# Optimization experiments

Measured on AMD Instinct MI355X. Metric: run time of the kernel, lower is better.

The kernel has to match this reference:

```python
import jax, jax.numpy as jnp
import numpy as np

IMG = 640.0
FISHER_EPS = 1e-6
BN_EPS = 1e-5
K = 100  # num_proposals

def _conv(x, w, b, stride=1, pad=1):
    y = jax.lax.conv_general_dilated(x, w, (stride, stride), [(pad, pad), (pad, pad)],
                                     dimension_numbers=('NCHW', 'OIHW', 'NCHW'))
    return y + b[None, :, None, None]

def _bn(x, g, b):
    # eval-mode BatchNorm, running_mean=0, running_var=1
    scale = g / np.float32(np.sqrt(1.0 + BN_EPS))
    return x * scale[None, :, None, None] + b[None, :, None, None]

def _lin(x, w, b):
    return jnp.einsum('...i,oi->...o', x, w) + b

def _gelu(x):
    return jax.nn.gelu(x, approximate=False)

def setup_inputs():
    key = jax.random.key(0)
    ks = iter(jax.random.split(key, 64))
    def W(shape, s=0.05):
        return (jax.random.normal(next(ks), shape) * s).astype(jnp.float32)
    Z = lambda n: jnp.zeros((n,), jnp.float32)
    O = lambda n: jnp.ones((n,), jnp.float32)
    return dict(
        images=jax.random.normal(next(ks), (8, 3, 640, 640), jnp.float32),
        enc_w1=W((32, 3, 3, 3)), enc_b1=Z(32), bn1_g=O(32), bn1_b=Z(32),
        enc_w2=W((64, 32, 3, 3)), enc_b2=Z(64), bn2_g=O(64), bn2_b=Z(64),
        enc_w3=W((128, 64, 3, 3)), enc_b3=Z(128), bn3_g=O(128), bn3_b=Z(128),
        dist_w1=W((64, 128, 3, 3)), dist_b1=Z(64), dist_w2=W((15, 64, 1, 1)), dist_b2=Z(15),
        feat_w=W((128, 128, 3, 3)), feat_b=Z(128), bnf_g=O(128), bnf_b=Z(128),
        temperature=jnp.array(1.0, jnp.float32),
        score_w1=W((64, 129, 3, 3)), score_b1=Z(64), score_w2=W((1, 64, 1, 1)), score_b2=Z(1),
        det_w=W((128, 128)), det_b=Z(128),
        co_w1=W((32, 128)), co_b1=Z(32), co_w2=W((2, 32)), co_b2=Z(2),
        sz_w1=W((32, 128)), sz_b1=Z(32), sz_w2=W((2, 32)), sz_b2=Z(2),
        an_w1=W((16, 128)), an_b1=Z(16), an_w2=W((1, 16)), an_b2=Z(1),
        cls_w1=W((64, 128)), cls_b1=Z(64), cls_w2=W((15, 64)), cls_b2=Z(15),
        conf_w1=W((16, 129)), conf_b1=Z(16), conf_w2=W((1, 16)), conf_b2=Z(1),
    )

def reference(images, enc_w1, enc_b1, bn1_g, bn1_b, enc_w2, enc_b2, bn2_g, bn2_b,
              enc_w3, enc_b3, bn3_g, bn3_b, dist_w1, dist_b1, dist_w2, dist_b2,
              feat_w, feat_b, bnf_g, bnf_b, temperature,
              score_w1, score_b1, score_w2, score_b2, det_w, det_b,
              co_w1, co_b1, co_w2, co_b2, sz_w1, sz_b1, sz_w2, sz_b2,
              an_w1, an_b1, an_w2, an_b2, cls_w1, cls_b1, cls_w2, cls_b2,
              conf_w1, conf_b1, conf_w2, conf_b2):
    # FisherEncoder
    x = _gelu(_bn(_conv(images, enc_w1, enc_b1, stride=2), bn1_g, bn1_b))
    x = _gelu(_bn(_conv(x, enc_w2, enc_b2, stride=2), bn2_g, bn2_b))
    enc = _gelu(_bn(_conv(x, enc_w3, enc_b3), bn3_g, bn3_b))
    logits = _conv(jax.nn.relu(_conv(enc, dist_w1, dist_b1)), dist_w2, dist_b2, pad=0)
    features = _gelu(_bn(_conv(enc, feat_w, feat_b), bnf_g, bnf_b))
    # DiagonalFisherModule (analytical; num_fisher_samples=0)
    temp = jnp.clip(temperature, 0.1, 10.0)
    probs = jax.nn.sigmoid(logits / temp)
    fisher_map = jnp.maximum(probs * (1.0 - probs), FISHER_EPS).sum(axis=1, keepdims=True)
    # score refinement
    score_in = jnp.concatenate([features, fisher_map], axis=1)
    scores_map = jax.nn.sigmoid(_conv(jax.nn.relu(_conv(score_in, score_w1, score_b1)), score_w2, score_b2, pad=0))
    B, C, H, W = features.shape
    N = H * W
    top_scores, top_idx = jax.lax.top_k(scores_map.reshape(B, N), K)  # (B,K)
    ys = (top_idx // W).astype(jnp.float32) / H
    xs = (top_idx % W).astype(jnp.float32) / W
    coords = jnp.stack([xs, ys], axis=-1)  # (B,K,2)
    # gather per-proposal features
    local = jnp.take_along_axis(features.reshape(B, C, N), top_idx[:, None, :], axis=2)  # (B,C,K)
    local = jnp.transpose(local, (0, 2, 1))  # (B,K,C)
    feat = jax.nn.relu(_lin(local, det_w, det_b))
    offsets = jnp.tanh(_lin(jax.nn.relu(_lin(feat, co_w1, co_b1)), co_w2, co_b2))
    offset_scale = jnp.array([1.0 / W, 1.0 / H], jnp.float32)
    centers = (coords + offsets * offset_scale) * IMG
    wh = jnp.exp(jnp.clip(_lin(jax.nn.relu(_lin(feat, sz_w1, sz_b1)), sz_w2, sz_b2), -5.0, 5.0)) * (IMG / 10.0)
    a = _lin(jax.nn.relu(_lin(feat, an_w1, an_b1)), an_w2, an_b2)
    angles = jnp.arctan2(jnp.sin(a), jnp.cos(a))
    cls_logits = _lin(jax.nn.relu(_lin(feat, cls_w1, cls_b1)), cls_w2, cls_b2)
    conf_in = jnp.concatenate([feat, top_scores[..., None]], axis=-1)
    conf = jax.nn.sigmoid(_lin(jax.nn.relu(_lin(conf_in, conf_w1, conf_b1)), conf_w2, conf_b2))
    return (centers, wh, angles, cls_logits, conf, top_scores, fisher_map)
```

## Files before the change

### kernel.cpp

```cpp
#include <hip/hip_runtime.h>
#include <cmath>

#define ACT_NONE 0
#define ACT_GELU 1
#define ACT_RELU 2

#define OFF_CENTERS 0
#define OFF_WH      1600
#define OFF_ANG     3200
#define OFF_CLS     4000
#define OFF_CONF    16000
#define OFF_TOPS    16800
#define OFF_FISH    17600

__device__ __forceinline__ float gelu_f(float v) {
    return 0.5f * v * (1.f + erff(v * 0.70710678118654752f));
}

__global__ void prep_weight(const float* __restrict__ w, const float* __restrict__ bn_g,
                            float* __restrict__ wt, int O, int I9) {
    int i = blockIdx.x * 256 + threadIdx.x;
    if (i >= O * I9) return;
    int o = i / I9, r = i % I9;
    float s = 1.f;
    if (bn_g) {
        double sq = sqrt(1.0 + 1e-5);
        s = bn_g[o] / (float)sq;
    }
    wt[(size_t)r * O + o] = w[(size_t)o * I9 + r] * s;
}

__global__ void prep_bias(const float* __restrict__ b, const float* __restrict__ bn_g,
                          const float* __restrict__ bn_b, float* __restrict__ outb, int O) {
    int o = blockIdx.x * 128 + threadIdx.x;
    if (o >= O) return;
    float s = 1.f, t = 0.f;
    if (bn_g) {
        double sq = sqrt(1.0 + 1e-5);
        s = bn_g[o] / (float)sq;
        t = bn_b[o];
    }
    outb[o] = b[o] * s + t;
}

__global__ void zero_cols_k(float* __restrict__ buf, int nplanes, int W, int H) {
    int i = blockIdx.x * 256 + threadIdx.x;
    if (i >= nplanes * H * 2) return;
    const int p = i / (H * 2), j = i % (H * 2);
    const int y = j >> 1, side = j & 1;
    buf[(size_t)p * W * H + (size_t)y * W + (side ? W - 1 : 0)] = 0.f;
}

__global__ void zero_fill_k(float* __restrict__ buf, int n) {
    int i = blockIdx.x * 256 + threadIdx.x;
    if (i < n) buf[i] = 0.f;
}

template<int CIN, int COUT, int CHUNK, int STRIDE, int HOUT, int WOUT, int ACT, bool OPADX>
__global__ __launch_bounds__(256) void conv3x3_k(
    const float* __restrict__ in, const float* __restrict__ wt,
    const float* __restrict__ bias, float* __restrict__ out)
{
    constexpr int HIN = HOUT * STRIDE, WIN = WOUT * STRIDE;
    constexpr int NCH = COUT / CHUNK;
    const int tx = threadIdx.x & 15, ty = threadIdx.x >> 4;
    const int x = blockIdx.x * 16 + tx;
    const int y = blockIdx.y * 16 + ty;
    const int b = blockIdx.z / NCH;
    const int co0 = (blockIdx.z % NCH) * CHUNK;

    float acc[CHUNK];
#pragma unroll
    for (int c = 0; c < CHUNK; ++c) acc[c] = bias[co0 + c];

    const float* inb = in + (size_t)b * CIN * HIN * WIN;
#pragma unroll 1
    for (int ci = 0; ci < CIN; ++ci) {
        const float* ip = inb + (size_t)ci * HIN * WIN;
#pragma unroll
        for (int ky = 0; ky < 3; ++ky) {
            const int iy = y * STRIDE + ky - 1;
            const bool yok = (unsigned)iy < (unsigned)HIN;
#pragma unroll
            for (int kx = 0; kx < 3; ++kx) {
                const int ix = x * STRIDE + kx - 1;
                const bool ok = yok && ((unsigned)ix < (unsigned)WIN);
                const float v = ok ? ip[(size_t)iy * WIN + ix] : 0.f;
                const float* wp = wt + ((size_t)(ci * 9 + ky * 3 + kx)) * COUT + co0;
#pragma unroll
                for (int c = 0; c < CHUNK; ++c) acc[c] = fmaf(v, wp[c], acc[c]);
            }
        }
    }
#pragma unroll
    for (int c = 0; c < CHUNK; ++c) {
        float v = acc[c];
        if (ACT == ACT_GELU) v = gelu_f(v);
        if (ACT == ACT_RELU) v = fmaxf(v, 0.f);
        if (OPADX) {
            out[((size_t)b * COUT + co0 + c) * (size_t)(HOUT * (WOUT + 2))
                + (size_t)y * (WOUT + 2) + (x + 1)] = v;
        } else {
            out[((size_t)b * COUT + co0 + c) * (size_t)(HOUT * WOUT)
                + (size_t)y * WOUT + x] = v;
        }
    }
}

#define FMA16(A, V, W0, W1, W2, W3) do { \
  A[0]=fmaf((V),(W0).x,A[0]); A[1]=fmaf((V),(W0).y,A[1]); A[2]=fmaf((V),(W0).z,A[2]); A[3]=fmaf((V),(W0).w,A[3]); \
  A[4]=fmaf((V),(W1).x,A[4]); A[5]=fmaf((V),(W1).y,A[5]); A[6]=fmaf((V),(W1).z,A[6]); A[7]=fmaf((V),(W1).w,A[7]); \
  A[8]=fmaf((V),(W2).x,A[8]); A[9]=fmaf((V),(W2).y,A[9]); A[10]=fmaf((V),(W2).z,A[10]); A[11]=fmaf((V),(W2).w,A[11]); \
  A[12]=fmaf((V),(W3).x,A[12]); A[13]=fmaf((V),(W3).y,A[13]); A[14]=fmaf((V),(W3).z,A[14]); A[15]=fmaf((V),(W3).w,A[15]); \
} while (0)

template<int CIN, int COUT, int S, int PW, int HIN, int ACT, bool EXTRA, bool OPAD>
__global__ __launch_bounds__(256) void conv4_k(
    const float* __restrict__ in, const float* __restrict__ extra,
    const float* __restrict__ wt, const float* __restrict__ bias,
    const float* __restrict__ zrow, float* __restrict__ out)
{
    constexpr int PPIN = HIN * PW;
    constexpr int CHUNK = 16, NCH = COUT / CHUNK;
    constexpr int CTOT = CIN + (EXTRA ? 1 : 0);
    constexpr int NL = 3 * S + 3;
    const int tx = threadIdx.x & 7, ty = threadIdx.x >> 3;
    const int ox0 = blockIdx.x * 32 + tx * 4;
    const int oy  = blockIdx.y * 32 + ty;
    const int b   = blockIdx.z / NCH;
    const int co0 = (blockIdx.z % NCH) * CHUNK;

    float acc[4][16];
#pragma unroll
    for (int c = 0; c < 16; ++c) {
        const float bv = bias[co0 + c];
#pragma unroll
        for (int p = 0; p < 4; ++p) acc[p][c] = bv;
    }

    int rowoff[3], rok[3];
#pragma unroll
    for (int r = 0; r < 3; ++r) {
        const int riy = oy * S + r - 1;
        rok[r] = (riy >= 0 && riy < HIN) ? 1 : 0;
        const int rr = riy < 0 ? 0 : (riy >= HIN ? HIN - 1 : riy);
        rowoff[r] = rr * PW + ox0 * S;
    }

    const float* inb = in + (size_t)b * CIN * PPIN;
    const float* wb  = wt + co0;

#pragma unroll 1
    for (int ci = 0; ci < CTOT; ++ci) {
        const float* chp = (EXTRA && ci == CIN) ? (extra + (size_t)b * PPIN)
                                                : (inb + (size_t)ci * PPIN);
        float v[3][NL];
#pragma unroll
        for (int r = 0; r < 3; ++r) {
            const float* pr = rok[r] ? (chp + rowoff[r]) : zrow;
#pragma unroll
            for (int j = 0; j < NL / 2; ++j) {
                const float2 t = *(const float2*)(pr + 2 * j);
                v[r][2 * j] = t.x; v[r][2 * j + 1] = t.y;
            }
            if (NL & 1) v[r][NL - 1] = pr[NL - 1];
        }
        const float* wr = wb + (size_t)(ci * 9) * COUT;
#pragma unroll
        for (int ky = 0; ky < 3; ++ky) {
#pragma unroll
            for (int kx = 0; kx < 3; ++kx) {
                const float* wp = wr + (size_t)(ky * 3 + kx) * COUT;
                const float4 w0 = *(const float4*)(wp);
                const float4 w1 = *(const float4*)(wp + 4);
                const float4 w2 = *(const float4*)(wp + 8);
                const float4 w3 = *(const float4*)(wp + 12);
#pragma unroll
                for (int p = 0; p < 4; ++p) {
                    const float a = v[ky][p * S + kx];
                    FMA16(acc[p], a, w0, w1, w2, w3);
                }
            }
        }
    }

#pragma unroll
    for (int c = 0; c < 16; ++c) {
#pragma unroll
        for (int p = 0; p < 4; ++p) {
            float u = acc[p][c];
            if (ACT == ACT_GELU) u = gelu_f(u);
            if (ACT == ACT_RELU) u = fmaxf(u, 0.f);
            if (OPAD) {
                out[((size_t)b * COUT + co0 + c) * (160 * 162)
                    + (size_t)oy * 162 + (ox0 + p + 1)] = u;
            } else {
                out[((size_t)b * COUT + co0 + c) * (160 * 160)
                    + (size_t)oy * 160 + (ox0 + p)] = u;
            }
        }
    }
}

__global__ __launch_bounds__(256) void dist2_fisher_k(
    const float* __restrict__ hid, const float* __restrict__ w ,
    const float* __restrict__ b2 , const float* __restrict__ temp,
    float* __restrict__ fisher_out, float* __restrict__ fisher_pad)
{
    const int p = blockIdx.x * 256 + threadIdx.x;
    if (p >= 8 * 25600) return;
    const int bi = p / 25600, pix = p % 25600;
    const float* h = hid + (size_t)bi * 64 * 25600 + pix;
    float hv[64];
#pragma unroll
    for (int i = 0; i < 64; ++i) hv[i] = h[(size_t)i * 25600];
    const float t = fminf(fmaxf(temp[0], 0.1f), 10.f);
    const float inv_t = 1.f / t;
    float fsum = 0.f;
#pragma unroll 1
    for (int c = 0; c < 15; ++c) {
        float l = b2[c];
        const float* wr = w + c * 64;
#pragma unroll
        for (int i = 0; i < 64; ++i) l = fmaf(hv[i], wr[i], l);
        const float pr = 1.f / (1.f + expf(-l * inv_t));
        fsum += fmaxf(pr * (1.f - pr), 1e-6f);
    }
    fisher_out[p] = fsum;
    const int yy = pix / 160, xx = pix % 160;
    fisher_pad[(size_t)bi * (160 * 162) + (size_t)yy * 162 + (xx + 1)] = fsum;
}

__global__ __launch_bounds__(256) void score2_k(
    const float* __restrict__ hid, const float* __restrict__ w ,
    const float* __restrict__ b, float* __restrict__ sc)
{
    const int p = blockIdx.x * 256 + threadIdx.x;
    if (p >= 8 * 25600) return;
    const int bi = p / 25600, pix = p % 25600;
    const float* h = hid + (size_t)bi * 64 * 25600 + pix;
    float a = b[0];
#pragma unroll
    for (int i = 0; i < 64; ++i) a = fmaf(h[(size_t)i * 25600], w[i], a);
    sc[p] = 1.f / (1.f + expf(-a));
}

#define TK_CAP 512
__global__ __launch_bounds__(256) void topk_radix_k(
    const float* __restrict__ scores, float* __restrict__ topv, int* __restrict__ topi)
{
    __shared__ unsigned hist[256];
    __shared__ unsigned gv[128]; __shared__ int gi[128];
    __shared__ unsigned ecnt[2];
    __shared__ int ei_[TK_CAP];
    __shared__ unsigned fv[100]; __shared__ int fi[100];
    __shared__ unsigned sel_prefix; __shared__ int sel_remaining;
    const int b = blockIdx.x, t = threadIdx.x;
    const float* s = scores + (size_t)b * 25600;

    unsigned prefix = 0; int remaining = 100;
    for (int pass = 0; pass < 4; ++pass) {
        const int shift = 24 - 8 * pass;
        hist[t] = 0;
        __syncthreads();
        const unsigned pmask = (pass == 0) ? 0u : (0xFFFFFFFFu << (shift + 8));
        for (int i = t; i < 25600; i += 256) {
            const unsigned k = __float_as_uint(s[i]);
            if ((k & pmask) == prefix)
                atomicAdd(&hist[(k >> shift) & 255], 1u);
        }
        __syncthreads();
        if (t == 0) {
            unsigned cum = 0; int bkt = 0;
            for (int d = 255; d >= 0; --d) {
                const unsigned c = hist[d];
                if (cum + c >= (unsigned)remaining) { bkt = d; break; }
                cum += c;
            }
            sel_prefix = prefix | ((unsigned)bkt << shift);
            sel_remaining = remaining - (int)cum;
        }
        __syncthreads();
        prefix = sel_prefix; remaining = sel_remaining;
        __syncthreads();
    }
    if (t == 0) { ecnt[0] = 0; ecnt[1] = 0; }
    __syncthreads();
    for (int i = t; i < 25600; i += 256) {
        const unsigned k = __float_as_uint(s[i]);
        if (k > prefix) {
            const unsigned p = atomicAdd(&ecnt[0], 1u);
            gv[p] = k; gi[p] = i;
        } else if (k == prefix) {
            const unsigned p = atomicAdd(&ecnt[1], 1u);
            if (p < TK_CAP) ei_[p] = i;
        }
    }
    __syncthreads();
    const int cG = (int)ecnt[0];
    const int cE = (int)ecnt[1] < TK_CAP ? (int)ecnt[1] : TK_CAP;
    if (t < cG) { fv[t] = gv[t]; fi[t] = gi[t]; }
    if (t < cE) {
        const int idx = ei_[t]; int r = 0;
        for (int l = 0; l < cE; ++l) r += (ei_[l] < idx) ? 1 : 0;
        if (r < remaining) { fv[cG + r] = prefix; fi[cG + r] = idx; }
    }
    __syncthreads();
    if (t < 100) {
        const unsigned myv = fv[t]; const int myi = fi[t]; int r = 0;
        for (int l = 0; l < 100; ++l) {
            const unsigned v = fv[l]; const int li = fi[l];
            r += (v > myv || (v == myv && li < myi)) ? 1 : 0;
        }
        topv[b * 100 + r] = __uint_as_float(myv);
        topi[b * 100 + r] = myi;
    }
}

__global__ __launch_bounds__(128) void heads_k(
    const float* __restrict__ features, const float* __restrict__ topv,
    const int* __restrict__ topi,
    const float* __restrict__ det_w, const float* __restrict__ det_b,
    const float* __restrict__ co_w1, const float* __restrict__ co_b1,
    const float* __restrict__ co_w2, const float* __restrict__ co_b2,
    const float* __restrict__ sz_w1, const float* __restrict__ sz_b1,
    const float* __restrict__ sz_w2, const float* __restrict__ sz_b2,
    const float* __restrict__ an_w1, const float* __restrict__ an_b1,
    const float* __restrict__ an_w2, const float* __restrict__ an_b2,
    const float* __restrict__ cls_w1, const float* __restrict__ cls_b1,
    const float* __restrict__ cls_w2, const float* __restrict__ cls_b2,
    const float* __restrict__ conf_w1, const float* __restrict__ conf_b1,
    const float* __restrict__ conf_w2, const float* __restrict__ conf_b2,
    float* __restrict__ out)
{
    __shared__ float local[128], feat[128], h[64];
    const int bk = blockIdx.x;
    const int b = bk / 100;
    const int t = threadIdx.x;
    const int idx = topi[bk];
    const float score = topv[bk];

    const int yy = idx / 160, xx = idx % 160;
    local[t] = features[((size_t)b * 128 + t) * (160 * 162) + (size_t)yy * 162 + (xx + 1)];
    __syncthreads();

    {
        float a = det_b[t];
        const float* wr = det_w + (size_t)t * 128;
#pragma unroll
        for (int i = 0; i < 128; ++i) a = fmaf(local[i], wr[i], a);
        feat[t] = fmaxf(a, 0.f);
    }
    __syncthreads();

    if (t < 32) {
        float a = co_b1[t];
        const float* wr = co_w1 + (size_t)t * 128;
#pragma unroll
        for (int i = 0; i < 128; ++i) a = fmaf(feat[i], wr[i], a);
        h[t] = fmaxf(a, 0.f);
    }
    __syncthreads();
    if (t < 2) {
        float a = co_b2[t];
        const float* wr = co_w2 + (size_t)t * 32;
#pragma unroll
        for (int j = 0; j < 32; ++j) a = fmaf(h[j], wr[j], a);
        const float off = tanhf(a);
        const float coord = (t == 0) ? (float)xx * (1.f / 160.f) : (float)yy * (1.f / 160.f);
        out[OFF_CENTERS + bk * 2 + t] = (coord + off * (1.f / 160.f)) * 640.f;
    }
    __syncthreads();

    if (t < 32) {
        float a = sz_b1[t];
        const float* wr = sz_w1 + (size_t)t * 128;
#pragma unroll
        for (int i = 0; i < 128; ++i) a = fmaf(feat[i], wr[i], a);
        h[t] = fmaxf(a, 0.f);
    }
    __syncthreads();
    if (t < 2) {
        float a = sz_b2[t];
        const float* wr = sz_w2 + (size_t)t * 32;
#pragma unroll
        for (int j = 0; j < 32; ++j) a = fmaf(h[j], wr[j], a);
        a = fminf(fmaxf(a, -5.f), 5.f);
        out[OFF_WH + bk * 2 + t] = expf(a) * 64.f;
    }
    __syncthreads();

    if (t < 16) {
        float a = an_b1[t];
        const float* wr = an_w1 + (size_t)t * 128;
#pragma unroll
        for (int i = 0; i < 128; ++i) a = fmaf(feat[i], wr[i], a);
        h[t] = fmaxf(a, 0.f);
    }
    __syncthreads();
    if (t == 0) {
        float a = an_b2[0];
#pragma unroll
        for (int j = 0; j < 16; ++j) a = fmaf(h[j], an_w2[j], a);
        out[OFF_ANG + bk] = atan2f(sinf(a), cosf(a));
    }
    __syncthreads();

    if (t < 64) {
        float a = cls_b1[t];
        const float* wr = cls_w1 + (size_t)t * 128;
#pragma unroll
        for (int i = 0; i < 128; ++i) a = fmaf(feat[i], wr[i], a);
        h[t] = fmaxf(a, 0.f);
    }
    __syncthreads();
    if (t < 15) {
        float a = cls_b2[t];
        const float* wr = cls_w2 + (size_t)t * 64;
#pragma unroll
        for (int j = 0; j < 64; ++j) a = fmaf(h[j], wr[j], a);
        out[OFF_CLS + bk * 15 + t] = a;
    }
    __syncthreads();

    if (t < 16) {
        float a = conf_b1[t];
        const float* wr = conf_w1 + (size_t)t * 129;
#pragma unroll
        for (int i = 0; i < 128; ++i) a = fmaf(feat[i], wr[i], a);
        a = fmaf(score, wr[128], a);
        h[t] = fmaxf(a, 0.f);
    }
    __syncthreads();
    if (t == 0) {
        float a = conf_b2[0];
#pragma unroll
        for (int j = 0; j < 16; ++j) a = fmaf(h[j], conf_w2[j], a);
        out[OFF_CONF + bk] = 1.f / (1.f + expf(-a));
    }
}

extern "C" void kernel_launch(void* const* d_in, const int* in_sizes, int n_in,
                              void* d_out, int out_size, void* d_ws, size_t ws_size,
                              hipStream_t stream)
{
    const float* images = (const float*)d_in[0];
    const float* enc_w1 = (const float*)d_in[1];
    const float* enc_b1 = (const float*)d_in[2];
    const float* bn1_g  = (const float*)d_in[3];
    const float* bn1_b  = (const float*)d_in[4];
    const float* enc_w2 = (const float*)d_in[5];
    const float* enc_b2 = (const float*)d_in[6];
    const float* bn2_g  = (const float*)d_in[7];
    const float* bn2_b  = (const float*)d_in[8];
    const float* enc_w3 = (const float*)d_in[9];
    const float* enc_b3 = (const float*)d_in[10];
    const float* bn3_g  = (const float*)d_in[11];
    const float* bn3_b  = (const float*)d_in[12];
    const float* dist_w1 = (const float*)d_in[13];
    const float* dist_b1 = (const float*)d_in[14];
    const float* dist_w2 = (const float*)d_in[15];
    const float* dist_b2 = (const float*)d_in[16];
    const float* feat_w = (const float*)d_in[17];
    const float* feat_b = (const float*)d_in[18];
    const float* bnf_g  = (const float*)d_in[19];
    const float* bnf_b  = (const float*)d_in[20];
    const float* temperature = (const float*)d_in[21];
    const float* score_w1 = (const float*)d_in[22];
    const float* score_b1 = (const float*)d_in[23];
    const float* score_w2 = (const float*)d_in[24];
    const float* score_b2 = (const float*)d_in[25];
    const float* det_w = (const float*)d_in[26];
    const float* det_b = (const float*)d_in[27];
    const float* co_w1 = (const float*)d_in[28];
    const float* co_b1 = (const float*)d_in[29];
    const float* co_w2 = (const float*)d_in[30];
    const float* co_b2 = (const float*)d_in[31];
    const float* sz_w1 = (const float*)d_in[32];
    const float* sz_b1 = (const float*)d_in[33];
    const float* sz_w2 = (const float*)d_in[34];
    const float* sz_b2 = (const float*)d_in[35];
    const float* an_w1 = (const float*)d_in[36];
    const float* an_b1 = (const float*)d_in[37];
    const float* an_w2 = (const float*)d_in[38];
    const float* an_b2 = (const float*)d_in[39];
    const float* cls_w1 = (const float*)d_in[40];
    const float* cls_b1 = (const float*)d_in[41];
    const float* cls_w2 = (const float*)d_in[42];
    const float* cls_b2 = (const float*)d_in[43];
    const float* conf_w1 = (const float*)d_in[44];
    const float* conf_b1 = (const float*)d_in[45];
    const float* conf_w2 = (const float*)d_in[46];
    const float* conf_b2 = (const float*)d_in[47];

    float* out = (float*)d_out;

    float* Wk = (float*)d_ws;
    size_t off = 0;
    auto alloc = [&](size_t n) { float* p = Wk + off; off += n; return p; };
    float* wt1 = alloc(27 * 32);    float* b1 = alloc(32);
    float* wt2 = alloc(288 * 64);   float* b2 = alloc(64);
    float* wt3 = alloc(576 * 128);  float* b3 = alloc(128);
    float* wtf = alloc(1152 * 128); float* bf = alloc(128);
    float* wtd = alloc(1152 * 64);
    float* wts = alloc(1161 * 64);
    float* zrow = alloc(32);
    float* slotA = alloc(26542080);
    float* slotB = alloc(13314560);
    float* slotC = alloc(26542080);
    float* fisher_pad = slotB + 13107200;
    float* scores = slotC;
    int*   topi   = (int*)(slotC + 204800);

    auto g256 = [](int n) { return dim3((n + 255) / 256); };

    prep_weight<<<g256(32 * 27), 256, 0, stream>>>(enc_w1, bn1_g, wt1, 32, 27);
    prep_bias<<<1, 128, 0, stream>>>(enc_b1, bn1_g, bn1_b, b1, 32);
    prep_weight<<<g256(64 * 288), 256, 0, stream>>>(enc_w2, bn2_g, wt2, 64, 288);
    prep_bias<<<1, 128, 0, stream>>>(enc_b2, bn2_g, bn2_b, b2, 64);
    prep_weight<<<g256(128 * 576), 256, 0, stream>>>(enc_w3, bn3_g, wt3, 128, 576);
    prep_bias<<<1, 128, 0, stream>>>(enc_b3, bn3_g, bn3_b, b3, 128);
    prep_weight<<<g256(128 * 1152), 256, 0, stream>>>(feat_w, bnf_g, wtf, 128, 1152);
    prep_bias<<<1, 128, 0, stream>>>(feat_b, bnf_g, bnf_b, bf, 128);
    prep_weight<<<g256(64 * 1152), 256, 0, stream>>>(dist_w1, nullptr, wtd, 64, 1152);
    prep_weight<<<g256(64 * 1161), 256, 0, stream>>>(score_w1, nullptr, wts, 64, 1161);

    zero_fill_k<<<1, 32, 0, stream>>>(zrow, 32);
    zero_cols_k<<<g256(256 * 320 * 2), 256, 0, stream>>>(slotA, 8 * 32, 322, 320);
    zero_cols_k<<<g256(512 * 160 * 2), 256, 0, stream>>>(slotB, 8 * 64, 162, 160);
    zero_cols_k<<<g256(1024 * 160 * 2), 256, 0, stream>>>(slotC, 8 * 128, 162, 160);

    conv3x3_k<3, 32, 32, 2, 320, 320, ACT_GELU, true>
        <<<dim3(20, 20, 8), 256, 0, stream>>>(images, wt1, b1, slotA);
    conv4_k<32, 64, 2, 322, 320, ACT_GELU, false, true>
        <<<dim3(5, 5, 8 * 4), 256, 0, stream>>>(slotA, nullptr, wt2, b2, zrow, slotB);
    zero_cols_k<<<g256(1024 * 160 * 2), 256, 0, stream>>>(slotA, 8 * 128, 162, 160);
    conv4_k<64, 128, 1, 162, 160, ACT_GELU, false, true>
        <<<dim3(5, 5, 8 * 8), 256, 0, stream>>>(slotB, nullptr, wt3, b3, zrow, slotC);

    conv4_k<128, 64, 1, 162, 160, ACT_RELU, false, false>
        <<<dim3(5, 5, 8 * 4), 256, 0, stream>>>(slotC, nullptr, wtd, dist_b1, zrow, slotB);
    zero_fill_k<<<g256(207360), 256, 0, stream>>>(fisher_pad, 207360);
    dist2_fisher_k<<<800, 256, 0, stream>>>(slotB, dist_w2, dist_b2, temperature,
                                            out + OFF_FISH, fisher_pad);

    conv4_k<128, 128, 1, 162, 160, ACT_GELU, false, true>
        <<<dim3(5, 5, 8 * 8), 256, 0, stream>>>(slotC, nullptr, wtf, bf, zrow, slotA);

    conv4_k<128, 64, 1, 162, 160, ACT_RELU, true, false>
        <<<dim3(5, 5, 8 * 4), 256, 0, stream>>>(slotA, fisher_pad, wts, score_b1, zrow, slotB);
    score2_k<<<800, 256, 0, stream>>>(slotB, score_w2, score_b2, scores);

    topk_radix_k<<<8, 256, 0, stream>>>(scores, out + OFF_TOPS, topi);

    heads_k<<<800, 128, 0, stream>>>(slotA, out + OFF_TOPS, topi,
                                     det_w, det_b, co_w1, co_b1, co_w2, co_b2,
                                     sz_w1, sz_b1, sz_w2, sz_b2,
                                     an_w1, an_b1, an_w2, an_b2,
                                     cls_w1, cls_b1, cls_w2, cls_b2,
                                     conf_w1, conf_b1, conf_w2, conf_b2, out);
    (void)in_sizes; (void)n_in; (void)out_size; (void)ws_size;
}
```

Baseline: 2.291 ms.

## Merge prep and padding-zero launches and double-buffer channel loads in conv4

The ten weight and bias preparation launches become one combined kernel, and the four padding-zero launches become a second one, which cuts launch overhead. Inside the conv4 kernel the per-channel input rows are now loaded one channel ahead into a second register set (v0/v1 ping-pong), so global loads overlap the FMA work on the current channel. The double buffer raises register pressure and may lower occupancy in the main convolution kernels.

Result: slower. 2.662 ms (+16.2%).

```diff
diff --git a/kernel.cpp b/kernel.cpp
--- a/kernel.cpp
+++ b/kernel.cpp
@@ -17,38 +17,65 @@
     return 0.5f * v * (1.f + erff(v * 0.70710678118654752f));
 }
 
-__global__ void prep_weight(const float* __restrict__ w, const float* __restrict__ bn_g,
-                            float* __restrict__ wt, int O, int I9) {
+__device__ __forceinline__ void wtr_seg(const float* __restrict__ w, const float* __restrict__ g,
+                                        float* __restrict__ dst, int O, int I9, int j) {
+    const int o = j / I9, r = j % I9;
+    float s = 1.f;
+    if (g) {
+        double sq = sqrt(1.0 + 1e-5);
+        s = g[o] / (float)sq;
+    }
+    dst[(size_t)r * O + o] = w[(size_t)o * I9 + r] * s;
+}
+__device__ __forceinline__ void btr_seg(const float* __restrict__ b, const float* __restrict__ g,
+                                        const float* __restrict__ bb, float* __restrict__ dst, int o) {
+    double sq = sqrt(1.0 + 1e-5);
+    const float s = g[o] / (float)sq;
+    dst[o] = b[o] * s + bb[o];
+}
+
+__global__ __launch_bounds__(256) void prep_all_k(
+    const float* ew1, const float* g1, const float* ew2, const float* g2,
+    const float* ew3, const float* g3, const float* fw,  const float* gf,
+    const float* dw,  const float* sw,
+    const float* eb1, const float* bb1, const float* eb2, const float* bb2,
+    const float* eb3, const float* bb3, const float* fb,  const float* bbf,
+    float* wt1, float* wt2, float* wt3, float* wtf, float* wtd, float* wts,
+    float* ob1, float* ob2, float* ob3, float* obf)
+{
     int i = blockIdx.x * 256 + threadIdx.x;
-    if (i >= O * I9) return;
-    int o = i / I9, r = i % I9;
-    float s = 1.f;
-    if (bn_g) {
-        double sq = sqrt(1.0 + 1e-5);
-        s = bn_g[o] / (float)sq;
-    }
-    wt[(size_t)r * O + o] = w[(size_t)o * I9 + r] * s;
-}
-
-__global__ void prep_bias(const float* __restrict__ b, const float* __restrict__ bn_g,
-                          const float* __restrict__ bn_b, float* __restrict__ outb, int O) {
-    int o = blockIdx.x * 128 + threadIdx.x;
-    if (o >= O) return;
-    float s = 1.f, t = 0.f;
-    if (bn_g) {
-        double sq = sqrt(1.0 + 1e-5);
-        s = bn_g[o] / (float)sq;
-        t = bn_b[o];
-    }
-    outb[o] = b[o] * s + t;
+    if (i < 864)    { wtr_seg(ew1, g1, wt1, 32, 27, i);    return; }  i -= 864;
+    if (i < 18432)  { wtr_seg(ew2, g2, wt2, 64, 288, i);   return; }  i -= 18432;
+    if (i < 73728)  { wtr_seg(ew3, g3, wt3, 128, 576, i);  return; }  i -= 73728;
+    if (i < 147456) { wtr_seg(fw,  gf, wtf, 128, 1152, i); return; }  i -= 147456;
+    if (i < 73728)  { wtr_seg(dw, nullptr, wtd, 64, 1152, i); return; } i -= 73728;
+    if (i < 74304)  { wtr_seg(sw, nullptr, wts, 64, 1161, i); return; } i -= 74304;
+    if (i < 32)     { btr_seg(eb1, g1, bb1, ob1, i); return; }  i -= 32;
+    if (i < 64)     { btr_seg(eb2, g2, bb2, ob2, i); return; }  i -= 64;
+    if (i < 128)    { btr_seg(eb3, g3, bb3, ob3, i); return; }  i -= 128;
+    if (i < 128)    { btr_seg(fb,  gf, bbf, obf, i); return; }
+}
+
+__device__ __forceinline__ void zcol(float* __restrict__ buf, int W, int H, int j) {
+    const int p = j / (H * 2), r = j % (H * 2);
+    const int y = r >> 1, side = r & 1;
+    buf[(size_t)p * W * H + (size_t)y * W + (side ? W - 1 : 0)] = 0.f;
+}
+
+__global__ __launch_bounds__(256) void zero_pads_k(
+    float* zrow, float* p1, float* p2, float* p3)
+{
+    int i = blockIdx.x * 256 + threadIdx.x;
+    if (i < 32) { zrow[i] = 0.f; return; }          i -= 32;
+    if (i < 256 * 320 * 2)  { zcol(p1, 322, 320, i); return; }  i -= 256 * 320 * 2;
+    if (i < 512 * 160 * 2)  { zcol(p2, 162, 160, i); return; }  i -= 512 * 160 * 2;
+    if (i < 1024 * 160 * 2) { zcol(p3, 162, 160, i); return; }
 }
 
 __global__ void zero_cols_k(float* __restrict__ buf, int nplanes, int W, int H) {
     int i = blockIdx.x * 256 + threadIdx.x;
     if (i >= nplanes * H * 2) return;
-    const int p = i / (H * 2), j = i % (H * 2);
-    const int y = j >> 1, side = j & 1;
-    buf[(size_t)p * W * H + (size_t)y * W + (side ? W - 1 : 0)] = 0.f;
+    zcol(buf, W, H, i);
 }
 
 __global__ void zero_fill_k(float* __restrict__ buf, int n) {
@@ -150,21 +177,23 @@
     const float* inb = in + (size_t)b * CIN * PPIN;
     const float* wb  = wt + co0;
 
-#pragma unroll 1
-    for (int ci = 0; ci < CTOT; ++ci) {
-        const float* chp = (EXTRA && ci == CIN) ? (extra + (size_t)b * PPIN)
-                                                : (inb + (size_t)ci * PPIN);
-        float v[3][NL];
+    auto chptr = [&](int ci) -> const float* {
+        return (EXTRA && ci == CIN) ? (extra + (size_t)b * PPIN)
+                                    : (inb + (size_t)ci * PPIN);
+    };
+    auto ldch = [&](const float* chp, float vv[3][NL]) {
 #pragma unroll
         for (int r = 0; r < 3; ++r) {
             const float* pr = rok[r] ? (chp + rowoff[r]) : zrow;
 #pragma unroll
             for (int j = 0; j < NL / 2; ++j) {
                 const float2 t = *(const float2*)(pr + 2 * j);
-                v[r][2 * j] = t.x; v[r][2 * j + 1] = t.y;
+                vv[r][2 * j] = t.x; vv[r][2 * j + 1] = t.y;
             }
-            if (NL & 1) v[r][NL - 1] = pr[NL - 1];
-        }
+            if (NL & 1) vv[r][NL - 1] = pr[NL - 1];
+        }
+    };
+    auto fmach = [&](const float vv[3][NL], int ci) {
         const float* wr = wb + (size_t)(ci * 9) * COUT;
 #pragma unroll
         for (int ky = 0; ky < 3; ++ky) {
@@ -177,10 +206,22 @@
                 const float4 w3 = *(const float4*)(wp + 12);
 #pragma unroll
                 for (int p = 0; p < 4; ++p) {
-                    const float a = v[ky][p * S + kx];
+                    const float a = vv[ky][p * S + kx];
                     FMA16(acc[p], a, w0, w1, w2, w3);
                 }
             }
+        }
+    };
+
+    float v0[3][NL], v1[3][NL];
+    ldch(chptr(0), v0);
+#pragma unroll 1
+    for (int ci = 0; ci < CTOT; ci += 2) {
+        if (ci + 1 < CTOT) ldch(chptr(ci + 1), v1);
+        fmach(v0, ci);
+        if (ci + 1 < CTOT) {
+            if (ci + 2 < CTOT) ldch(chptr(ci + 2), v0);
+            fmach(v1, ci + 1);
         }
     }
 
@@ -514,21 +555,12 @@
 
     auto g256 = [](int n) { return dim3((n + 255) / 256); };
 
-    prep_weight<<<g256(32 * 27), 256, 0, stream>>>(enc_w1, bn1_g, wt1, 32, 27);
-    prep_bias<<<1, 128, 0, stream>>>(enc_b1, bn1_g, bn1_b, b1, 32);
-    prep_weight<<<g256(64 * 288), 256, 0, stream>>>(enc_w2, bn2_g, wt2, 64, 288);
-    prep_bias<<<1, 128, 0, stream>>>(enc_b2, bn2_g, bn2_b, b2, 64);
-    prep_weight<<<g256(128 * 576), 256, 0, stream>>>(enc_w3, bn3_g, wt3, 128, 576);
-    prep_bias<<<1, 128, 0, stream>>>(enc_b3, bn3_g, bn3_b, b3, 128);
-    prep_weight<<<g256(128 * 1152), 256, 0, stream>>>(feat_w, bnf_g, wtf, 128, 1152);
-    prep_bias<<<1, 128, 0, stream>>>(feat_b, bnf_g, bnf_b, bf, 128);
-    prep_weight<<<g256(64 * 1152), 256, 0, stream>>>(dist_w1, nullptr, wtd, 64, 1152);
-    prep_weight<<<g256(64 * 1161), 256, 0, stream>>>(score_w1, nullptr, wts, 64, 1161);
-
-    zero_fill_k<<<1, 32, 0, stream>>>(zrow, 32);
-    zero_cols_k<<<g256(256 * 320 * 2), 256, 0, stream>>>(slotA, 8 * 32, 322, 320);
-    zero_cols_k<<<g256(512 * 160 * 2), 256, 0, stream>>>(slotB, 8 * 64, 162, 160);
-    zero_cols_k<<<g256(1024 * 160 * 2), 256, 0, stream>>>(slotC, 8 * 128, 162, 160);
+    prep_all_k<<<g256(388864), 256, 0, stream>>>(
+        enc_w1, bn1_g, enc_w2, bn2_g, enc_w3, bn3_g, feat_w, bnf_g,
+        dist_w1, score_w1,
+        enc_b1, bn1_b, enc_b2, bn2_b, enc_b3, bn3_b, feat_b, bnf_b,
+        wt1, wt2, wt3, wtf, wtd, wts, b1, b2, b3, bf);
+    zero_pads_k<<<g256(655392), 256, 0, stream>>>(zrow, slotA, slotB, slotC);
 
     conv3x3_k<3, 32, 32, 2, 320, 320, ACT_GELU, true>
         <<<dim3(20, 20, 8), 256, 0, stream>>>(images, wt1, b1, slotA);
```
